# Kernel optimization log

Hardware: AMD Instinct MI355X
Metric: run time of the kernel (lower is better)

## Reference

```python
import jax, jax.numpy as jnp
import numpy as np

H = 8  # head_number
NEG = -1e30


def setup_inputs() -> dict:
    key = jax.random.key(0)
    ks = jax.random.split(key, 12)
    B, D, L = 32, 1024, 1024
    s = 1.0 / np.sqrt(D)
    x = jax.random.normal(ks[0], (B, D, L), dtype=jnp.float32)
    mask = jax.random.randint(ks[1], (B, L), 0, 2, dtype=jnp.int32)
    wq = jax.random.normal(ks[2], (D, D), dtype=jnp.float32) * s
    bq = jnp.zeros((D,), dtype=jnp.float32)
    wk = jax.random.normal(ks[3], (D, D), dtype=jnp.float32) * s
    bk = jnp.zeros((D,), dtype=jnp.float32)
    wv = jax.random.normal(ks[4], (D, D), dtype=jnp.float32) * s
    bv = jnp.zeros((D,), dtype=jnp.float32)
    wo = jax.random.normal(ks[5], (D, D), dtype=jnp.float32) * s
    bo = jnp.zeros((D,), dtype=jnp.float32)
    return {"x": x, "mask": mask, "wq": wq, "bq": bq, "wk": wk, "bk": bk,
            "wv": wv, "bv": bv, "wo": wo, "bo": bo}


def reference(x, mask, wq, bq, wk, bk, wv, bv, wo, bo):
    # x: [B, D, L]; mask: [B, L] with 1 = masked (pad). Dropout in eval mode (identity).
    B, D, L = x.shape
    dh = D // H
    scale = 1.0 / np.sqrt(dh)
    xt = jnp.swapaxes(x, 1, 2)  # [B, L, D]
    q = (xt @ wq.T + bq).reshape(B, L, H, dh)
    k = (xt @ wk.T + bk).reshape(B, L, H, dh)
    v = (xt @ wv.T + bv).reshape(B, L, H, dh)
    scores = jnp.einsum('bqhd,bkhd->bhqk', q, k) * scale  # [B, H, L, L]
    m = mask.astype(scores.dtype)[:, None, None, :]  # broadcast over heads, query pos
    scores = scores * (1.0 - m) + m * NEG
    attn = jax.nn.softmax(scores, axis=-1)
    out = jnp.einsum('bhqk,bkhd->bqhd', attn, v).reshape(B, L, D)
    out = out @ wo.T + bo
    return jnp.swapaxes(out, 1, 2)  # [B, D, L]
```

## Files before the change

kernel.cpp:

```cpp
#include <hip/hip_runtime.h>
#include <hip/hip_bf16.h>

typedef __bf16 bf16_t;
typedef bf16_t bf16x8 __attribute__((ext_vector_type(8)));
typedef float f32x4 __attribute__((ext_vector_type(4)));

#define MFMA16(a, b, c) __builtin_amdgcn_mfma_f32_16x16x32_bf16(a, b, c, 0, 0, 0)
#define NEGV -1e30f

__device__ __forceinline__ unsigned short f2bf(float f) {
  union { float f; unsigned int u; } v; v.f = f;
  unsigned int r = v.u + 0x7FFFu + ((v.u >> 16) & 1u);
  return (unsigned short)(r >> 16);
}

__device__ __forceinline__ void gload16(const unsigned short* g, unsigned short* l) {
  __builtin_amdgcn_global_load_lds(
      (const __attribute__((address_space(1))) void*)g,
      (__attribute__((address_space(3))) void*)l, 16, 0, 0);
}

__global__ __launch_bounds__(256) void x_transpose(
    const float* __restrict__ x, unsigned short* __restrict__ xT)
{
  const int b = blockIdx.z;
  const int l0 = blockIdx.x * 64, d0 = blockIdx.y * 64;
  __shared__ __align__(16) unsigned short T[64][68];
  const int tid = threadIdx.x;
  const int dl = tid >> 4, lc = (tid & 15) * 4;
#pragma unroll
  for (int rep = 0; rep < 4; ++rep) {
    int d = dl + rep * 16;
    float4 v = *reinterpret_cast<const float4*>(
        x + ((size_t)b * 1024 + d0 + d) * 1024 + l0 + lc);
    ushort4 u;
    u.x = f2bf(v.x); u.y = f2bf(v.y); u.z = f2bf(v.z); u.w = f2bf(v.w);
    *reinterpret_cast<ushort4*>(&T[d][lc]) = u;
  }
  __syncthreads();
  const int dbase = (tid & 15) * 4, lbase = (tid >> 4) * 4;
  ushort4 r0 = *reinterpret_cast<const ushort4*>(&T[dbase + 0][lbase]);
  ushort4 r1 = *reinterpret_cast<const ushort4*>(&T[dbase + 1][lbase]);
  ushort4 r2 = *reinterpret_cast<const ushort4*>(&T[dbase + 2][lbase]);
  ushort4 r3 = *reinterpret_cast<const ushort4*>(&T[dbase + 3][lbase]);
  ushort4 w0 = {r0.x, r1.x, r2.x, r3.x};
  ushort4 w1 = {r0.y, r1.y, r2.y, r3.y};
  ushort4 w2 = {r0.z, r1.z, r2.z, r3.z};
  ushort4 w3 = {r0.w, r1.w, r2.w, r3.w};
  unsigned short* op = xT + ((size_t)b * 1024 + l0 + lbase) * 1024 + d0 + dbase;
  *reinterpret_cast<ushort4*>(op) = w0;
  *reinterpret_cast<ushort4*>(op + 1024) = w1;
  *reinterpret_cast<ushort4*>(op + 2048) = w2;
  *reinterpret_cast<ushort4*>(op + 3072) = w3;
}

__global__ __launch_bounds__(256) void w_convert(
    const float* __restrict__ wq, const float* __restrict__ wk,
    const float* __restrict__ wv, const float* __restrict__ wo,
    unsigned short* __restrict__ Wqkv, unsigned short* __restrict__ Wo)
{
  const int z = blockIdx.y;
  const float* src = (z == 0) ? wq : (z == 1) ? wk : (z == 2) ? wv : wo;
  unsigned short* dst = (z < 3) ? Wqkv + (size_t)z * 1048576 : Wo;
  size_t off = ((size_t)blockIdx.x * 256 + threadIdx.x) * 4;
  float4 v = *reinterpret_cast<const float4*>(src + off);
  ushort4 u = {f2bf(v.x), f2bf(v.y), f2bf(v.z), f2bf(v.w)};
  *reinterpret_cast<ushort4*>(dst + off) = u;
}

__global__ __launch_bounds__(512, 2) void qkv_gemm8(
    const unsigned short* __restrict__ xT, const unsigned short* __restrict__ Wqkv,
    const float* __restrict__ bq, const float* __restrict__ bk, const float* __restrict__ bv,
    unsigned short* __restrict__ Q, unsigned short* __restrict__ K,
    unsigned short* __restrict__ Vt)
{
  __shared__ __align__(16) unsigned short lds[2][4][8192];

  const int tid = threadIdx.x;
  const int wave = tid >> 6, lane = tid & 63;
  const int lr = lane & 15, lg = lane >> 4;
  const int wr = wave >> 2, wc = wave & 3;

  const int bid = blockIdx.x;
  const int swz = (bid & 7) * 192 + (bid >> 3);
  const int mt = swz / 12, nt = swz % 12;
  const int m0 = mt * 256, n0 = nt * 256;

  const unsigned short* Ag = xT + (size_t)m0 * 1024;
  const unsigned short* Bg = Wqkv + (size_t)n0 * 1024;

  const int srow = tid >> 2;
  const int schk = (tid & 3) * 8;

#define STAGE_HT(BUF, REG, TI)                                                 \
  {                                                                            \
    const int kt_ = ((TI) < 16 ? (TI) : 15) * 64 + (((REG)&1) * 32) + schk;    \
    const unsigned short* gp_ = (((REG) < 2) ? Ag : Bg);                       \
    _Pragma("unroll")                                                          \
    for (int j_ = 0; j_ < 2; ++j_)                                             \
      gload16(gp_ + (size_t)(j_ * 128 + srow) * 1024 + kt_,                    \
              &lds[BUF][REG][j_ * 4096 + tid * 8]);                            \
  }

#define LDA(BUF, KK, MH, AR)                                                   \
  _Pragma("unroll")                                                            \
  for (int mi_ = 0; mi_ < 4; ++mi_)                                            \
    AR[mi_] = *reinterpret_cast<const bf16x8*>(                                \
        &lds[BUF][KK][(wr * 128 + (MH)*64 + mi_ * 16 + lr) * 32 + lg * 8]);

#define LDB(BUF, KK, BR)                                                       \
  _Pragma("unroll")                                                            \
  for (int n_ = 0; n_ < 4; ++n_)                                               \
    BR[n_] = *reinterpret_cast<const bf16x8*>(                                 \
        &lds[BUF][2 + (KK)][(wc * 64 + n_ * 16 + lr) * 32 + lg * 8]);

#define MM(AR, BR, MH)                                                         \
  __builtin_amdgcn_s_setprio(1);                                               \
  _Pragma("unroll")                                                            \
  for (int mi_ = 0; mi_ < 4; ++mi_)                                            \
    _Pragma("unroll")                                                          \
    for (int n_ = 0; n_ < 4; ++n_)                                             \
      acc[(MH)*4 + mi_][n_] = MFMA16(AR[mi_], BR[n_], acc[(MH)*4 + mi_][n_]);  \
  __builtin_amdgcn_s_setprio(0);

#define BAR()                                                                  \
  {                                                                            \
    asm volatile("" ::: "memory");                                             \
    __builtin_amdgcn_s_barrier();                                              \
    asm volatile("" ::: "memory");                                             \
  }
#define VMW() asm volatile("s_waitcnt vmcnt(10)" ::: "memory")

  f32x4 acc[8][4];
#pragma unroll
  for (int m = 0; m < 8; ++m)
#pragma unroll
    for (int n = 0; n < 4; ++n) acc[m][n] = (f32x4){0.f, 0.f, 0.f, 0.f};

  STAGE_HT(0, 2, 0); STAGE_HT(0, 0, 0); STAGE_HT(0, 3, 0); STAGE_HT(0, 1, 0);
  STAGE_HT(1, 2, 1); STAGE_HT(1, 0, 1); STAGE_HT(1, 3, 1);
  VMW();
  BAR();

  for (int it = 0; it < 8; ++it) {
    const int T = 2 * it;
    bf16x8 a0[4], a1[4], b0[4], b1[4];
    LDB(0, 0, b0); LDA(0, 0, 0, a0);
    STAGE_HT(1, 1, T + 1);
    BAR();
    MM(a0, b0, 0);
    BAR();
    LDA(0, 0, 1, a1);
    STAGE_HT(0, 2, T + 2);
    BAR();
    MM(a1, b0, 1);
    VMW(); BAR();
    LDB(0, 1, b1); LDA(0, 1, 0, a0);
    STAGE_HT(0, 0, T + 2);
    BAR();
    MM(a0, b1, 0);
    BAR();
    LDA(0, 1, 1, a1);
    STAGE_HT(0, 3, T + 2);
    BAR();
    MM(a1, b1, 1);
    VMW(); BAR();
    LDB(1, 0, b0); LDA(1, 0, 0, a0);
    STAGE_HT(0, 1, T + 2);
    BAR();
    MM(a0, b0, 0);
    BAR();
    LDA(1, 0, 1, a1);
    STAGE_HT(1, 2, T + 3);
    BAR();
    MM(a1, b0, 1);
    VMW(); BAR();
    LDB(1, 1, b1); LDA(1, 1, 0, a0);
    STAGE_HT(1, 0, T + 3);
    BAR();
    MM(a0, b1, 0);
    BAR();
    LDA(1, 1, 1, a1);
    STAGE_HT(1, 3, T + 3);
    BAR();
    MM(a1, b1, 1);
    VMW(); BAR();
  }

  const int zi = n0 >> 10;
  const float* bias = (zi == 0) ? bq : (zi == 1) ? bk : bv;
  const int b = m0 >> 10;
  const int lbase = (m0 & 1023) + wr * 128;

  if (zi < 2) {
    unsigned short* op = ((zi == 0) ? Q : K);
#pragma unroll
    for (int n = 0; n < 4; ++n) {
      const int col = (n0 & 1023) + wc * 64 + n * 16 + lr;
      const int h = col >> 7, d = col & 127;
      const float bs = bias[col];
      unsigned short* hp = op + ((size_t)b * 8 + h) * 131072 + d;
#pragma unroll
      for (int m = 0; m < 8; ++m)
#pragma unroll
        for (int ii = 0; ii < 4; ++ii) {
          int l = lbase + m * 16 + lg * 4 + ii;
          hp[(size_t)l * 128] = f2bf(acc[m][n][ii] + bs);
        }
    }
  } else {
#pragma unroll
    for (int n = 0; n < 4; ++n) {
      const int col = (n0 & 1023) + wc * 64 + n * 16 + lr;
      const int h = col >> 7, d = col & 127;
      const float bs = bias[col];
      unsigned short* hp = Vt + ((size_t)b * 8 + h) * 131072 + (size_t)d * 1024;
#pragma unroll
      for (int m = 0; m < 8; ++m) {
        int l = lbase + m * 16 + lg * 4;
        ushort4 u = {f2bf(acc[m][n][0] + bs), f2bf(acc[m][n][1] + bs),
                     f2bf(acc[m][n][2] + bs), f2bf(acc[m][n][3] + bs)};
        *reinterpret_cast<ushort4*>(&hp[l]) = u;
      }
    }
  }
#undef STAGE_HT
#undef LDA
#undef LDB
#undef MM
#undef BAR
#undef VMW
}

__global__ __launch_bounds__(256) void out_gemm(
    const unsigned short* __restrict__ Wo, const unsigned short* __restrict__ O,
    const float* __restrict__ bo, float* __restrict__ out)
{
  const int tid = threadIdx.x;
  const int wave = tid >> 6, lane = tid & 63;
  const int lr = lane & 15, lg = lane >> 4;
  const int wr = wave >> 1, wc = wave & 1;
  const int mt = blockIdx.x & 7, nt = blockIdx.x >> 3;
  const int b = blockIdx.y;
  const int d0 = mt * 128, l0 = nt * 128;
  const unsigned short* Ap = Wo + (size_t)d0 * 1024;

  __shared__ __align__(16) unsigned short lA[128 * 64];
  __shared__ __align__(16) unsigned short lB[128 * 64];

  f32x4 acc[4][4];
#pragma unroll
  for (int m = 0; m < 4; ++m)
#pragma unroll
    for (int n = 0; n < 4; ++n) acc[m][n] = (f32x4){0.f, 0.f, 0.f, 0.f};

  const int srow = tid >> 3, scol = (tid & 7) * 8;

  for (int k0 = 0; k0 < 1024; k0 += 64) {
    const unsigned short* Bp =
        O + (((size_t)b * 8 + (k0 >> 7)) * 1024 + l0) * 128 + (k0 & 64);
#pragma unroll
    for (int i = 0; i < 4; ++i) {
      gload16(Ap + (size_t)(i * 32 + srow) * 1024 + k0 + scol, &lA[i * 2048 + tid * 8]);
      gload16(Bp + (size_t)(i * 32 + srow) * 128 + scol, &lB[i * 2048 + tid * 8]);
    }
    __syncthreads();
    bf16x8 af[2][4], bfr[2][4];
#pragma unroll
    for (int kk = 0; kk < 2; ++kk) {
#pragma unroll
      for (int m = 0; m < 4; ++m)
        af[kk][m] = *reinterpret_cast<const bf16x8*>(
            &lA[(wr * 64 + m * 16 + lr) * 64 + kk * 32 + lg * 8]);
#pragma unroll
      for (int n = 0; n < 4; ++n)
        bfr[kk][n] = *reinterpret_cast<const bf16x8*>(
            &lB[(wc * 64 + n * 16 + lr) * 64 + kk * 32 + lg * 8]);
    }
#pragma unroll
    for (int kk = 0; kk < 2; ++kk)
#pragma unroll
      for (int m = 0; m < 4; ++m)
#pragma unroll
        for (int n = 0; n < 4; ++n)
          acc[m][n] = MFMA16(af[kk][m], bfr[kk][n], acc[m][n]);
    __syncthreads();
  }

#pragma unroll
  for (int m = 0; m < 4; ++m) {
#pragma unroll
    for (int ii = 0; ii < 4; ++ii) {
      int dr = d0 + wr * 64 + m * 16 + lg * 4 + ii;
      float bs = bo[dr];
      float* orow = out + ((size_t)b * 1024 + dr) * 1024 + l0 + wc * 64 + lr;
#pragma unroll
      for (int n = 0; n < 4; ++n)
        orow[n * 16] = acc[m][n][ii] + bs;
    }
  }
}

__global__ __launch_bounds__(256) void flash_attn(
    const unsigned short* __restrict__ Q, const unsigned short* __restrict__ Kb,
    const unsigned short* __restrict__ Vt, const int* __restrict__ mask,
    unsigned short* __restrict__ O)
{
  const int tid = threadIdx.x, wave = tid >> 6, lane = tid & 63;
  const int lr = lane & 15, lg = lane >> 4;
  const int qt = blockIdx.x, h = blockIdx.y, b = blockIdx.z;
  const size_t bh = (size_t)b * 8 + h;
  const unsigned short* Qp = Q + bh * 131072;
  const unsigned short* Kp = Kb + bh * 131072;
  const unsigned short* Vp = Vt + bh * 131072;
  unsigned short* Op = O + bh * 131072;
  const int q0 = qt * 64 + wave * 16;
  const float SC2 = 0.12751744f;
  const float NEG2 = -1.442695e30f;

  __shared__ __align__(16) unsigned short Kl[2][64 * 128];
  __shared__ __align__(16) unsigned short Vl[2][128 * 64];
  __shared__ __align__(16) unsigned short plds[4][16 * 72];
  __shared__ float pen[1024];

  {
    const int4 mv = *reinterpret_cast<const int4*>(mask + b * 1024 + tid * 4);
    float4 pv;
    pv.x = mv.x ? NEG2 : 0.f; pv.y = mv.y ? NEG2 : 0.f;
    pv.z = mv.z ? NEG2 : 0.f; pv.w = mv.w ? NEG2 : 0.f;
    *reinterpret_cast<float4*>(&pen[tid * 4]) = pv;
  }

  unsigned short* myP = plds[wave];

  bf16x8 aq[4];
#pragma unroll
  for (int c = 0; c < 4; ++c)
    aq[c] = *reinterpret_cast<const bf16x8*>(&Qp[(size_t)(q0 + lr) * 128 + c * 32 + lg * 8]);

  const int ks_row = (tid >> 4);
  const int ks_cb0 = (tid & 15) * 16;
  const int vs_row = (tid >> 3);
  const int vs_cb0 = (tid & 7) * 16;

#define STAGE(bufi, ktv)                                                        \
  {                                                                             \
    _Pragma("unroll")                                                           \
    for (int i = 0; i < 4; ++i) {                                               \
      int krow = i * 16 + ks_row;                                               \
      int kcb = ks_cb0 ^ ((krow & 7) << 4);                                     \
      gload16(Kp + (size_t)((ktv) + krow) * 128 + (kcb >> 1),                   \
              &Kl[bufi][i * 2048 + wave * 512]);                                \
      int vrow = i * 32 + vs_row;                                               \
      int vcb = vs_cb0 ^ ((vrow & 7) << 4);                                     \
      gload16(Vp + (size_t)vrow * 1024 + (ktv) + (vcb >> 1),                    \
              &Vl[bufi][i * 2048 + wave * 512]);                                \
    }                                                                           \
  }

  f32x4 oacc[8];
#pragma unroll
  for (int dt = 0; dt < 8; ++dt) oacc[dt] = (f32x4){0.f, 0.f, 0.f, 0.f};
  float mrun = -3.0e38f;
  float lrun = 0.f;

  STAGE(0, 0);
  __syncthreads();

  int cur = 0;
  for (int t = 0; t < 16; ++t) {
    const int kt = t * 64;
    if (t < 15) STAGE(cur ^ 1, kt + 64);

    f32x4 s[4];
    __builtin_amdgcn_s_setprio(1);
#pragma unroll
    for (int n = 0; n < 4; ++n) {
      f32x4 a = (f32x4){0.f, 0.f, 0.f, 0.f};
      const int krow = n * 16 + lr;
      const int rsw = (krow & 7) << 4;
#pragma unroll
      for (int c = 0; c < 4; ++c) {
        bf16x8 bk = *reinterpret_cast<const bf16x8*>(
            &Kl[cur][krow * 128 + (((c * 64 + lg * 16) ^ rsw) >> 1)]);
        a = MFMA16(bk, aq[c], a);
      }
      s[n] = a;
    }
    __builtin_amdgcn_s_setprio(0);

#pragma unroll
    for (int n = 0; n < 4; ++n) {
      f32x4 pv = *reinterpret_cast<const f32x4*>(&pen[kt + n * 16 + lg * 4]);
#pragma unroll
      for (int i = 0; i < 4; ++i) s[n][i] = s[n][i] * SC2 + pv[i];
    }

    float mn[4];
#pragma unroll
    for (int n = 0; n < 4; ++n)
      mn[n] = fmaxf(fmaxf(s[n][0], s[n][1]), fmaxf(s[n][2], s[n][3]));
    float mx = fmaxf(fmaxf(mn[0], mn[1]), fmaxf(mn[2], mn[3]));
    mx = fmaxf(mx, __shfl_xor(mx, 16));
    mx = fmaxf(mx, __shfl_xor(mx, 32));

    if (!__all(mx <= mrun + 8.0f)) {
      float mnew = fmaxf(mrun, mx);
      float scq = __builtin_amdgcn_exp2f(mrun - mnew);
      mrun = mnew;
      lrun *= scq;
#pragma unroll
      for (int i = 0; i < 4; ++i) {
        float sco = __shfl(scq, lg * 4 + i);
#pragma unroll
        for (int dt = 0; dt < 8; ++dt) oacc[dt][i] *= sco;
      }
    }

    float p[4][4], lsn[4];
#pragma unroll
    for (int n = 0; n < 4; ++n) {
#pragma unroll
      for (int i = 0; i < 4; ++i)
        p[n][i] = __builtin_amdgcn_exp2f(s[n][i] - mrun);
      lsn[n] = (p[n][0] + p[n][1]) + (p[n][2] + p[n][3]);
    }
    float ls = (lsn[0] + lsn[1]) + (lsn[2] + lsn[3]);
    ls += __shfl_xor(ls, 16);
    ls += __shfl_xor(ls, 32);
    lrun += ls;

#pragma unroll
    for (int n = 0; n < 4; ++n)
#pragma unroll
      for (int t2 = 0; t2 < 2; ++t2) {
        unsigned int u;
        asm("v_cvt_pk_bf16_f32 %0, %1, %2"
            : "=v"(u) : "v"(p[n][2 * t2]), "v"(p[n][2 * t2 + 1]));
        *reinterpret_cast<unsigned int*>(
            &myP[lr * 72 + n * 16 + lg * 4 + t2 * 2]) = u;
      }
    bf16x8 pa0 = *reinterpret_cast<const bf16x8*>(&myP[lr * 72 + lg * 8]);
    bf16x8 pa1 = *reinterpret_cast<const bf16x8*>(&myP[lr * 72 + 32 + lg * 8]);

    __builtin_amdgcn_s_setprio(1);
#pragma unroll
    for (int dt = 0; dt < 8; ++dt) {
      const int vrow = dt * 16 + lr;
      const int rsw = (vrow & 7) << 4;
      bf16x8 bv0 = *reinterpret_cast<const bf16x8*>(
          &Vl[cur][vrow * 64 + (((lg * 16) ^ rsw) >> 1)]);
      bf16x8 bv1 = *reinterpret_cast<const bf16x8*>(
          &Vl[cur][vrow * 64 + (((64 + lg * 16) ^ rsw) >> 1)]);
      oacc[dt] = MFMA16(pa0, bv0, oacc[dt]);
      oacc[dt] = MFMA16(pa1, bv1, oacc[dt]);
    }
    __builtin_amdgcn_s_setprio(0);

    __syncthreads();
    cur ^= 1;
  }

  float linv[4];
#pragma unroll
  for (int i = 0; i < 4; ++i) {
    float lq = __shfl(lrun, lg * 4 + i);
    linv[i] = 1.0f / lq;
  }
#pragma unroll
  for (int dt = 0; dt < 8; ++dt)
#pragma unroll
    for (int i = 0; i < 4; ++i)
      Op[(size_t)(q0 + lg * 4 + i) * 128 + dt * 16 + lr] = f2bf(oacc[dt][i] * linv[i]);
}

__global__ __launch_bounds__(256) void qkv_proj_old(
    const float* __restrict__ x,
    const float* __restrict__ wq, const float* __restrict__ wk, const float* __restrict__ wv,
    const float* __restrict__ bq, const float* __restrict__ bk, const float* __restrict__ bv,
    unsigned short* __restrict__ Q, unsigned short* __restrict__ K, unsigned short* __restrict__ Vt)
{
  const int tid = threadIdx.x;
  const int wave = tid >> 6, lane = tid & 63;
  const int lr = lane & 15, lg = lane >> 4;
  const int wr = wave >> 1, wc = wave & 1;
  const int mt = blockIdx.x & 7, nt = blockIdx.x >> 3;
  const int b = blockIdx.y, z = blockIdx.z;
  const int l0 = mt * 128, i0 = nt * 128;
  const float* w    = (z == 0) ? wq : (z == 1) ? wk : wv;
  const float* bias = (z == 0) ? bq : (z == 1) ? bk : bv;
  unsigned short* outp = (z == 0) ? Q : (z == 1) ? K : Vt;

  __shared__ __align__(16) unsigned short lA[128 * 40];
  __shared__ __align__(16) unsigned short lB[128 * 40];

  f32x4 acc[4][4];
#pragma unroll
  for (int m = 0; m < 4; ++m)
#pragma unroll
    for (int n = 0; n < 4; ++n) acc[m][n] = (f32x4){0.f, 0.f, 0.f, 0.f};

  const int ad = tid >> 3, aj = tid & 7;
  const int br = tid >> 1, bh2 = tid & 1;

  for (int k0 = 0; k0 < 1024; k0 += 32) {
    const float* xp = x + ((size_t)b * 1024 + k0 + ad) * 1024 + l0;
#pragma unroll
    for (int rep = 0; rep < 4; ++rep) {
      float4 v = *reinterpret_cast<const float4*>(xp + aj * 4 + rep * 32);
      int lb = aj * 4 + rep * 32;
      lA[(lb + 0) * 40 + ad] = f2bf(v.x);
      lA[(lb + 1) * 40 + ad] = f2bf(v.y);
      lA[(lb + 2) * 40 + ad] = f2bf(v.z);
      lA[(lb + 3) * 40 + ad] = f2bf(v.w);
    }
    const float* wp = w + (size_t)(i0 + br) * 1024 + k0 + bh2 * 16;
#pragma unroll
    for (int rep = 0; rep < 4; ++rep) {
      float4 v = *reinterpret_cast<const float4*>(wp + rep * 4);
      int cb = br * 40 + bh2 * 16 + rep * 4;
      lB[cb + 0] = f2bf(v.x); lB[cb + 1] = f2bf(v.y);
      lB[cb + 2] = f2bf(v.z); lB[cb + 3] = f2bf(v.w);
    }
    __syncthreads();
    bf16x8 af[4], bfr[4];
#pragma unroll
    for (int m = 0; m < 4; ++m)
      af[m] = *reinterpret_cast<const bf16x8*>(&lA[(wr * 64 + m * 16 + lr) * 40 + lg * 8]);
#pragma unroll
    for (int n = 0; n < 4; ++n)
      bfr[n] = *reinterpret_cast<const bf16x8*>(&lB[(wc * 64 + n * 16 + lr) * 40 + lg * 8]);
#pragma unroll
    for (int m = 0; m < 4; ++m)
#pragma unroll
      for (int n = 0; n < 4; ++n)
        acc[m][n] = MFMA16(af[m], bfr[n], acc[m][n]);
    __syncthreads();
  }
#pragma unroll
  for (int n = 0; n < 4; ++n) {
    int col = i0 + wc * 64 + n * 16 + lr;
    float bs = bias[col];
    int h = col >> 7, d = col & 127;
#pragma unroll
    for (int m = 0; m < 4; ++m) {
#pragma unroll
      for (int ii = 0; ii < 4; ++ii) {
        int row = l0 + wr * 64 + m * 16 + lg * 4 + ii;
        unsigned short val = f2bf(acc[m][n][ii] + bs);
        if (z < 2)
          outp[(((size_t)b * 8 + h) * 1024 + row) * 128 + d] = val;
        else
          outp[(((size_t)b * 8 + h) * 128 + d) * 1024 + row] = val;
      }
    }
  }
}

__global__ __launch_bounds__(256) void out_proj_old(
    const unsigned short* __restrict__ Obuf, const float* __restrict__ wo,
    const float* __restrict__ bo, float* __restrict__ out)
{
  const int tid = threadIdx.x, wave = tid >> 6, lane = tid & 63;
  const int lr = lane & 15, lg = lane >> 4;
  const int wr = wave >> 1, wc = wave & 1;
  const int mt = blockIdx.x & 7, nt = blockIdx.x >> 3;
  const int b = blockIdx.y;
  const int d0 = mt * 128, l0 = nt * 128;

  __shared__ __align__(16) unsigned short lA[128 * 40];
  __shared__ __align__(16) unsigned short lB[128 * 40];

  f32x4 acc[4][4];
#pragma unroll
  for (int m = 0; m < 4; ++m)
#pragma unroll
    for (int n = 0; n < 4; ++n) acc[m][n] = (f32x4){0.f, 0.f, 0.f, 0.f};

  const int ar = tid >> 1, ah = tid & 1;

  for (int k0 = 0; k0 < 1024; k0 += 32) {
    const float* wp = wo + (size_t)(d0 + ar) * 1024 + k0 + ah * 16;
#pragma unroll
    for (int rep = 0; rep < 4; ++rep) {
      float4 v = *reinterpret_cast<const float4*>(wp + rep * 4);
      int cb = ar * 40 + ah * 16 + rep * 4;
      lA[cb + 0] = f2bf(v.x); lA[cb + 1] = f2bf(v.y);
      lA[cb + 2] = f2bf(v.z); lA[cb + 3] = f2bf(v.w);
    }
    {
      int head = k0 >> 7, dk = (k0 & 127) + ah * 16;
      const unsigned short* op =
          Obuf + (((size_t)b * 8 + head) * 1024 + l0 + ar) * 128 + dk;
#pragma unroll
      for (int rep = 0; rep < 2; ++rep) {
        bf16x8 v = *reinterpret_cast<const bf16x8*>(op + rep * 8);
        *reinterpret_cast<bf16x8*>(&lB[ar * 40 + ah * 16 + rep * 8]) = v;
      }
    }
    __syncthreads();
    bf16x8 af[4], bfr[4];
#pragma unroll
    for (int m = 0; m < 4; ++m)
      af[m] = *reinterpret_cast<const bf16x8*>(&lA[(wr * 64 + m * 16 + lr) * 40 + lg * 8]);
#pragma unroll
    for (int n = 0; n < 4; ++n)
      bfr[n] = *reinterpret_cast<const bf16x8*>(&lB[(wc * 64 + n * 16 + lr) * 40 + lg * 8]);
#pragma unroll
    for (int m = 0; m < 4; ++m)
#pragma unroll
      for (int n = 0; n < 4; ++n)
        acc[m][n] = MFMA16(af[m], bfr[n], acc[m][n]);
    __syncthreads();
  }
#pragma unroll
  for (int m = 0; m < 4; ++m) {
#pragma unroll
    for (int ii = 0; ii < 4; ++ii) {
      int dr = d0 + wr * 64 + m * 16 + lg * 4 + ii;
      float bs = bo[dr];
      float* orow = out + ((size_t)b * 1024 + dr) * 1024 + l0 + wc * 64 + lr;
#pragma unroll
      for (int n = 0; n < 4; ++n)
        orow[n * 16] = acc[m][n][ii] + bs;
    }
  }
}

extern "C" void kernel_launch(void* const* d_in, const int* in_sizes, int n_in,
                              void* d_out, int out_size, void* d_ws, size_t ws_size,
                              hipStream_t stream) {
  const float* x  = (const float*)d_in[0];
  const int* mask = (const int*)d_in[1];
  const float* wq = (const float*)d_in[2];
  const float* bq = (const float*)d_in[3];
  const float* wk = (const float*)d_in[4];
  const float* bk = (const float*)d_in[5];
  const float* wv = (const float*)d_in[6];
  const float* bv = (const float*)d_in[7];
  const float* wo = (const float*)d_in[8];
  const float* bo = (const float*)d_in[9];
  float* out = (float*)d_out;

  const size_t MB64 = (size_t)64 << 20;
  const size_t NEED = (size_t)264 << 20;

  if (ws_size >= NEED) {
    unsigned short* xT   = (unsigned short*)d_ws;
    unsigned short* Q    = (unsigned short*)((char*)d_ws + MB64);
    unsigned short* K    = (unsigned short*)((char*)d_ws + 2 * MB64);
    unsigned short* Vt   = (unsigned short*)((char*)d_ws + 3 * MB64);
    unsigned short* Wqkv = (unsigned short*)((char*)d_ws + 4 * MB64);
    unsigned short* Wo   = Wqkv + (size_t)3 * 1048576;

    x_transpose<<<dim3(16, 16, 32), 256, 0, stream>>>(x, xT);
    w_convert<<<dim3(1024, 4), 256, 0, stream>>>(wq, wk, wv, wo, Wqkv, Wo);
    qkv_gemm8<<<dim3(1536), 512, 0, stream>>>(xT, Wqkv, bq, bk, bv, Q, K, Vt);
    flash_attn<<<dim3(16, 8, 32), 256, 0, stream>>>(Q, K, Vt, mask, Q);
    out_gemm<<<dim3(64, 32), 256, 0, stream>>>(Wo, Q, bo, out);
  } else {
    unsigned short* Q  = (unsigned short*)d_ws;
    unsigned short* K  = Q + (size_t)33554432;
    unsigned short* Vt = K + (size_t)33554432;
    qkv_proj_old<<<dim3(64, 32, 3), 256, 0, stream>>>(x, wq, wk, wv, bq, bk, bv, Q, K, Vt);
    flash_attn<<<dim3(16, 8, 32), 256, 0, stream>>>(Q, K, Vt, mask, Q);
    out_proj_old<<<dim3(64, 32), 256, 0, stream>>>(Q, wo, bo, out);
  }
}
```

Measured before the change: 660.6 us.

## Add 256x256 pipelined output GEMM and shrink flash-attention KV tile to 32

Replaces the simple 128x128 output-projection GEMM with a 512-thread, 256x256-tile kernel. It reuses the qkv_gemm8 multi-stage LDS pipeline macros and swizzles block order for better reuse of Wo and O. Separately, flash attention now steps over 32-key tiles instead of 64, with a new V LDS swizzle and a smaller P buffer. The goal is less LDS use and more occupancy, at the cost of twice as many loop iterations and barriers.

Result: no change. 652.4 us (-1.2%).

```diff
diff --git a/kernel.cpp b/kernel.cpp
--- a/kernel.cpp
+++ b/kernel.cpp
@@ -225,80 +225,123 @@
     }
   }
 #undef STAGE_HT
+}
+
+__global__ __launch_bounds__(512, 2) void out_gemm8(
+    const unsigned short* __restrict__ Wo, const unsigned short* __restrict__ O,
+    const float* __restrict__ bo, float* __restrict__ out)
+{
+  __shared__ __align__(16) unsigned short lds[2][4][8192];
+
+  const int tid = threadIdx.x;
+  const int wave = tid >> 6, lane = tid & 63;
+  const int lr = lane & 15, lg = lane >> 4;
+  const int wr = wave >> 2, wc = wave & 3;
+
+  const int b = blockIdx.y;
+  const int bid = blockIdx.x;
+  const int swz = (bid & 7) * 2 + (bid >> 3);
+  const int mt = swz >> 2, nt = swz & 3;
+  const int d0 = mt * 256, l0 = nt * 256;
+
+  const unsigned short* Ag = Wo + (size_t)d0 * 1024;
+  const unsigned short* Og = O + (size_t)b * 8 * 131072;
+
+  const int srow = tid >> 2;
+  const int schk = (tid & 3) * 8;
+
+#define STAGE_HT(BUF, REG, TI)                                                 \
+  {                                                                            \
+    const int kt_ = ((TI) < 16 ? (TI) : 15) * 64 + (((REG)&1) * 32) + schk;    \
+    if ((REG) < 2) {                                                           \
+      _Pragma("unroll")                                                        \
+      for (int j_ = 0; j_ < 2; ++j_)                                           \
+        gload16(Ag + (size_t)(j_ * 128 + srow) * 1024 + kt_,                   \
+                &lds[BUF][REG][j_ * 4096 + tid * 8]);                          \
+    } else {                                                                   \
+      const int h_ = kt_ >> 7, dk_ = kt_ & 127;                                \
+      _Pragma("unroll")                                                        \
+      for (int j_ = 0; j_ < 2; ++j_)                                           \
+        gload16(Og + (size_t)h_ * 131072 +                                     \
+                    (size_t)(l0 + j_ * 128 + srow) * 128 + dk_,                \
+                &lds[BUF][REG][j_ * 4096 + tid * 8]);                          \
+    }                                                                          \
+  }
+
+  f32x4 acc[8][4];
+#pragma unroll
+  for (int m = 0; m < 8; ++m)
+#pragma unroll
+    for (int n = 0; n < 4; ++n) acc[m][n] = (f32x4){0.f, 0.f, 0.f, 0.f};
+
+  STAGE_HT(0, 2, 0); STAGE_HT(0, 0, 0); STAGE_HT(0, 3, 0); STAGE_HT(0, 1, 0);
+  STAGE_HT(1, 2, 1); STAGE_HT(1, 0, 1); STAGE_HT(1, 3, 1);
+  VMW();
+  BAR();
+
+  for (int it = 0; it < 8; ++it) {
+    const int T = 2 * it;
+    bf16x8 a0[4], a1[4], b0[4], b1[4];
+    LDB(0, 0, b0); LDA(0, 0, 0, a0);
+    STAGE_HT(1, 1, T + 1);
+    BAR();
+    MM(a0, b0, 0);
+    BAR();
+    LDA(0, 0, 1, a1);
+    STAGE_HT(0, 2, T + 2);
+    BAR();
+    MM(a1, b0, 1);
+    VMW(); BAR();
+    LDB(0, 1, b1); LDA(0, 1, 0, a0);
+    STAGE_HT(0, 0, T + 2);
+    BAR();
+    MM(a0, b1, 0);
+    BAR();
+    LDA(0, 1, 1, a1);
+    STAGE_HT(0, 3, T + 2);
+    BAR();
+    MM(a1, b1, 1);
+    VMW(); BAR();
+    LDB(1, 0, b0); LDA(1, 0, 0, a0);
+    STAGE_HT(0, 1, T + 2);
+    BAR();
+    MM(a0, b0, 0);
+    BAR();
+    LDA(1, 0, 1, a1);
+    STAGE_HT(1, 2, T + 3);
+    BAR();
+    MM(a1, b0, 1);
+    VMW(); BAR();
+    LDB(1, 1, b1); LDA(1, 1, 0, a0);
+    STAGE_HT(1, 0, T + 3);
+    BAR();
+    MM(a0, b1, 0);
+    BAR();
+    LDA(1, 1, 1, a1);
+    STAGE_HT(1, 3, T + 3);
+    BAR();
+    MM(a1, b1, 1);
+    VMW(); BAR();
+  }
+
+#pragma unroll
+  for (int m = 0; m < 8; ++m) {
+#pragma unroll
+    for (int ii = 0; ii < 4; ++ii) {
+      int dr = d0 + wr * 128 + m * 16 + lg * 4 + ii;
+      float bs = bo[dr];
+      float* orow = out + ((size_t)b * 1024 + dr) * 1024 + l0 + wc * 64 + lr;
+#pragma unroll
+      for (int n = 0; n < 4; ++n)
+        orow[n * 16] = acc[m][n][ii] + bs;
+    }
+  }
+#undef STAGE_HT
 #undef LDA
 #undef LDB
 #undef MM
 #undef BAR
 #undef VMW
-}
-
-__global__ __launch_bounds__(256) void out_gemm(
-    const unsigned short* __restrict__ Wo, const unsigned short* __restrict__ O,
-    const float* __restrict__ bo, float* __restrict__ out)
-{
-  const int tid = threadIdx.x;
-  const int wave = tid >> 6, lane = tid & 63;
-  const int lr = lane & 15, lg = lane >> 4;
-  const int wr = wave >> 1, wc = wave & 1;
-  const int mt = blockIdx.x & 7, nt = blockIdx.x >> 3;
-  const int b = blockIdx.y;
-  const int d0 = mt * 128, l0 = nt * 128;
-  const unsigned short* Ap = Wo + (size_t)d0 * 1024;
-
-  __shared__ __align__(16) unsigned short lA[128 * 64];
-  __shared__ __align__(16) unsigned short lB[128 * 64];
-
-  f32x4 acc[4][4];
-#pragma unroll
-  for (int m = 0; m < 4; ++m)
-#pragma unroll
-    for (int n = 0; n < 4; ++n) acc[m][n] = (f32x4){0.f, 0.f, 0.f, 0.f};
-
-  const int srow = tid >> 3, scol = (tid & 7) * 8;
-
-  for (int k0 = 0; k0 < 1024; k0 += 64) {
-    const unsigned short* Bp =
-        O + (((size_t)b * 8 + (k0 >> 7)) * 1024 + l0) * 128 + (k0 & 64);
-#pragma unroll
-    for (int i = 0; i < 4; ++i) {
-      gload16(Ap + (size_t)(i * 32 + srow) * 1024 + k0 + scol, &lA[i * 2048 + tid * 8]);
-      gload16(Bp + (size_t)(i * 32 + srow) * 128 + scol, &lB[i * 2048 + tid * 8]);
-    }
-    __syncthreads();
-    bf16x8 af[2][4], bfr[2][4];
-#pragma unroll
-    for (int kk = 0; kk < 2; ++kk) {
-#pragma unroll
-      for (int m = 0; m < 4; ++m)
-        af[kk][m] = *reinterpret_cast<const bf16x8*>(
-            &lA[(wr * 64 + m * 16 + lr) * 64 + kk * 32 + lg * 8]);
-#pragma unroll
-      for (int n = 0; n < 4; ++n)
-        bfr[kk][n] = *reinterpret_cast<const bf16x8*>(
-            &lB[(wc * 64 + n * 16 + lr) * 64 + kk * 32 + lg * 8]);
-    }
-#pragma unroll
-    for (int kk = 0; kk < 2; ++kk)
-#pragma unroll
-      for (int m = 0; m < 4; ++m)
-#pragma unroll
-        for (int n = 0; n < 4; ++n)
-          acc[m][n] = MFMA16(af[kk][m], bfr[kk][n], acc[m][n]);
-    __syncthreads();
-  }
-
-#pragma unroll
-  for (int m = 0; m < 4; ++m) {
-#pragma unroll
-    for (int ii = 0; ii < 4; ++ii) {
-      int dr = d0 + wr * 64 + m * 16 + lg * 4 + ii;
-      float bs = bo[dr];
-      float* orow = out + ((size_t)b * 1024 + dr) * 1024 + l0 + wc * 64 + lr;
-#pragma unroll
-      for (int n = 0; n < 4; ++n)
-        orow[n * 16] = acc[m][n][ii] + bs;
-    }
-  }
 }
 
 __global__ __launch_bounds__(256) void flash_attn(
@@ -318,9 +361,9 @@
   const float SC2 = 0.12751744f;
   const float NEG2 = -1.442695e30f;
 
-  __shared__ __align__(16) unsigned short Kl[2][64 * 128];
-  __shared__ __align__(16) unsigned short Vl[2][128 * 64];
-  __shared__ __align__(16) unsigned short plds[4][16 * 72];
+  __shared__ __align__(16) unsigned short Kl[2][4096];
+  __shared__ __align__(16) unsigned short Vl[2][4096];
+  __shared__ __align__(16) unsigned short plds[4][16 * 40];
   __shared__ float pen[1024];
 
   {
@@ -338,23 +381,19 @@
   for (int c = 0; c < 4; ++c)
     aq[c] = *reinterpret_cast<const bf16x8*>(&Qp[(size_t)(q0 + lr) * 128 + c * 32 + lg * 8]);
 
-  const int ks_row = (tid >> 4);
-  const int ks_cb0 = (tid & 15) * 16;
-  const int vs_row = (tid >> 3);
-  const int vs_cb0 = (tid & 7) * 16;
-
 #define STAGE(bufi, ktv)                                                        \
   {                                                                             \
     _Pragma("unroll")                                                           \
-    for (int i = 0; i < 4; ++i) {                                               \
-      int krow = i * 16 + ks_row;                                               \
-      int kcb = ks_cb0 ^ ((krow & 7) << 4);                                     \
+    for (int i = 0; i < 2; ++i) {                                               \
+      int krow = i * 16 + (tid >> 4);                                           \
+      int kcb = ((tid & 15) * 16) ^ ((krow & 7) << 4);                          \
       gload16(Kp + (size_t)((ktv) + krow) * 128 + (kcb >> 1),                   \
-              &Kl[bufi][i * 2048 + wave * 512]);                                \
-      int vrow = i * 32 + vs_row;                                               \
-      int vcb = vs_cb0 ^ ((vrow & 7) << 4);                                     \
-      gload16(Vp + (size_t)vrow * 1024 + (ktv) + (vcb >> 1),                    \
-              &Vl[bufi][i * 2048 + wave * 512]);                                \
+              &Kl[bufi][i * 2048 + tid * 8]);                                   \
+      int aoff = i * 4096 + tid * 16;                                           \
+      int r_ = aoff >> 6;                                                       \
+      int Lb = aoff ^ (((r_ ^ (r_ >> 2)) & 3) << 4);                            \
+      gload16(Vp + (size_t)(Lb >> 6) * 1024 + (ktv) + ((Lb & 63) >> 1),         \
+              &Vl[bufi][i * 2048 + tid * 8]);                                   \
     }                                                                           \
   }
 
@@ -368,14 +407,14 @@
   __syncthreads();
 
   int cur = 0;
-  for (int t = 0; t < 16; ++t) {
-    const int kt = t * 64;
-    if (t < 15) STAGE(cur ^ 1, kt + 64);
-
-    f32x4 s[4];
+  for (int t = 0; t < 32; ++t) {
+    const int kt = t * 32;
+    if (t < 31) STAGE(cur ^ 1, kt + 32);
+
+    f32x4 s[2];
     __builtin_amdgcn_s_setprio(1);
 #pragma unroll
-    for (int n = 0; n < 4; ++n) {
+    for (int n = 0; n < 2; ++n) {
       f32x4 a = (f32x4){0.f, 0.f, 0.f, 0.f};
       const int krow = n * 16 + lr;
       const int rsw = (krow & 7) << 4;
@@ -390,17 +429,14 @@
     __builtin_amdgcn_s_setprio(0);
 
 #pragma unroll
-    for (int n = 0; n < 4; ++n) {
+    for (int n = 0; n < 2; ++n) {
       f32x4 pv = *reinterpret_cast<const f32x4*>(&pen[kt + n * 16 + lg * 4]);
 #pragma unroll
       for (int i = 0; i < 4; ++i) s[n][i] = s[n][i] * SC2 + pv[i];
     }
 
-    float mn[4];
-#pragma unroll
-    for (int n = 0; n < 4; ++n)
-      mn[n] = fmaxf(fmaxf(s[n][0], s[n][1]), fmaxf(s[n][2], s[n][3]));
-    float mx = fmaxf(fmaxf(mn[0], mn[1]), fmaxf(mn[2], mn[3]));
+    float mx = fmaxf(fmaxf(fmaxf(s[0][0], s[0][1]), fmaxf(s[0][2], s[0][3])),
+                     fmaxf(fmaxf(s[1][0], s[1][1]), fmaxf(s[1][2], s[1][3])));
     mx = fmaxf(mx, __shfl_xor(mx, 16));
     mx = fmaxf(mx, __shfl_xor(mx, 32));
 
@@ -417,43 +453,38 @@
       }
     }
 
-    float p[4][4], lsn[4];
-#pragma unroll
-    for (int n = 0; n < 4; ++n) {
+    float p[2][4];
+#pragma unroll
+    for (int n = 0; n < 2; ++n)
 #pragma unroll
       for (int i = 0; i < 4; ++i)
         p[n][i] = __builtin_amdgcn_exp2f(s[n][i] - mrun);
-      lsn[n] = (p[n][0] + p[n][1]) + (p[n][2] + p[n][3]);
-    }
-    float ls = (lsn[0] + lsn[1]) + (lsn[2] + lsn[3]);
+    float ls = ((p[0][0] + p[0][1]) + (p[0][2] + p[0][3])) +
+               ((p[1][0] + p[1][1]) + (p[1][2] + p[1][3]));
     ls += __shfl_xor(ls, 16);
     ls += __shfl_xor(ls, 32);
     lrun += ls;
 
 #pragma unroll
-    for (int n = 0; n < 4; ++n)
+    for (int n = 0; n < 2; ++n)
 #pragma unroll
       for (int t2 = 0; t2 < 2; ++t2) {
         unsigned int u;
         asm("v_cvt_pk_bf16_f32 %0, %1, %2"
             : "=v"(u) : "v"(p[n][2 * t2]), "v"(p[n][2 * t2 + 1]));
         *reinterpret_cast<unsigned int*>(
-            &myP[lr * 72 + n * 16 + lg * 4 + t2 * 2]) = u;
+            &myP[lr * 40 + n * 16 + lg * 4 + t2 * 2]) = u;
       }
-    bf16x8 pa0 = *reinterpret_cast<const bf16x8*>(&myP[lr * 72 + lg * 8]);
-    bf16x8 pa1 = *reinterpret_cast<const bf16x8*>(&myP[lr * 72 + 32 + lg * 8]);
+    bf16x8 pa0 = *reinterpret_cast<const bf16x8*>(&myP[lr * 40 + lg * 8]);
 
     __builtin_amdgcn_s_setprio(1);
 #pragma unroll
     for (int dt = 0; dt < 8; ++dt) {
-      const int vrow = dt * 16 + lr;
-      const int rsw = (vrow & 7) << 4;
-      bf16x8 bv0 = *reinterpret_cast<const bf16x8*>(
-          &Vl[cur][vrow * 64 + (((lg * 16) ^ rsw) >> 1)]);
-      bf16x8 bv1 = *reinterpret_cast<const bf16x8*>(
-          &Vl[cur][vrow * 64 + (((64 + lg * 16) ^ rsw) >> 1)]);
-      oacc[dt] = MFMA16(pa0, bv0, oacc[dt]);
-      oacc[dt] = MFMA16(pa1, bv1, oacc[dt]);
+      const int rr = dt * 16 + lr;
+      const int aL = rr * 64 + lg * 16;
+      const int ph = aL ^ (((rr ^ (rr >> 2)) & 3) << 4);
+      bf16x8 bv = *reinterpret_cast<const bf16x8*>(&Vl[cur][ph >> 1]);
+      oacc[dt] = MFMA16(pa0, bv, oacc[dt]);
     }
     __builtin_amdgcn_s_setprio(0);
 
@@ -472,6 +503,7 @@
 #pragma unroll
     for (int i = 0; i < 4; ++i)
       Op[(size_t)(q0 + lg * 4 + i) * 128 + dt * 16 + lr] = f2bf(oacc[dt][i] * linv[i]);
+#undef STAGE
 }
 
 __global__ __launch_bounds__(256) void qkv_proj_old(
@@ -657,7 +689,7 @@
     w_convert<<<dim3(1024, 4), 256, 0, stream>>>(wq, wk, wv, wo, Wqkv, Wo);
     qkv_gemm8<<<dim3(1536), 512, 0, stream>>>(xT, Wqkv, bq, bk, bv, Q, K, Vt);
     flash_attn<<<dim3(16, 8, 32), 256, 0, stream>>>(Q, K, Vt, mask, Q);
-    out_gemm<<<dim3(64, 32), 256, 0, stream>>>(Wo, Q, bo, out);
+    out_gemm8<<<dim3(16, 32), 512, 0, stream>>>(Wo, Q, bo, out);
   } else {
     unsigned short* Q  = (unsigned short*)d_ws;
     unsigned short* K  = Q + (size_t)33554432;
```
